# Kernel tuning notes

Hardware: AMD Instinct MI355X
Metric: run time of the kernel (lower is better)

Reference implementation:

```python
import jax, jax.numpy as jnp
import numpy as np

MID = 16
HEADS = 8
HEAD_DIM = MID // HEADS  # 2
EPS = 1e-5


def posembed(length, dim):
    # get_posembed_linear: sin-cos 1D positional embedding
    pos = jnp.arange(length, dtype=jnp.float32)
    omega = jnp.arange(dim // 2, dtype=jnp.float32) / (dim / 2.0)
    omega = 1.0 / (10000.0 ** omega)
    out = pos[:, None] * omega[None, :]  # [L, dim//2]
    return jnp.concatenate([jnp.sin(out), jnp.cos(out)], axis=1)  # [L, dim]


def layernorm(x, g, b):
    m = x.mean(-1, keepdims=True)
    v = ((x - m) ** 2).mean(-1, keepdims=True)
    return (x - m) * jax.lax.rsqrt(v + EPS) * g + b


def conv2d(x, w, b):
    # NCHW 3x3 SAME conv
    y = jax.lax.conv_general_dilated(x, w, (1, 1), 'SAME',
                                     dimension_numbers=('NCHW', 'OIHW', 'NCHW'))
    return y + b[None, :, None, None]


def attention(x, wq, wk, wv, wo, bo):
    # diffusers Attention: self-attn, no qkv bias, out bias
    B, S, C = x.shape
    q = (x @ wq.T).reshape(B, S, HEADS, HEAD_DIM)
    k = (x @ wk.T).reshape(B, S, HEADS, HEAD_DIM)
    v = (x @ wv.T).reshape(B, S, HEADS, HEAD_DIM)
    scale = 1.0 / np.sqrt(HEAD_DIM).astype(np.float32)
    scores = jnp.einsum('bshd,bthd->bhst', q, k) * scale
    p = jax.nn.softmax(scores, axis=-1)
    o = jnp.einsum('bhst,bthd->bshd', p, v).reshape(B, S, C)
    return o @ wo.T + bo


def setup_inputs() -> dict:
    key = jax.random.key(0)
    ks = jax.random.split(key, 24)

    def n(k, shape, s=0.05):
        return jax.random.normal(k, shape, dtype=jnp.float32) * s

    b, f, h, w, c = 2, 16, 64, 64, 16
    inp = {
        'hidden_states': n(ks[0], (b, f, h, w, c), 1.0),
        'ref_stats': n(ks[1], (b, f, h, w, c), 1.0),
        'emb': n(ks[2], (b, 512), 1.0),
        'conv_in_w': n(ks[3], (MID, c, 3, 3)),
        'conv_in_b': jnp.zeros((MID,), jnp.float32),
        'emb1_w': n(ks[4], (MID, 512)),
        'emb1_b': jnp.zeros((MID,), jnp.float32),
        'emb2_w': n(ks[5], (MID, MID)),
        'emb2_b': jnp.zeros((MID,), jnp.float32),
        'wqx': n(ks[6], (MID, MID)), 'wkx': n(ks[7], (MID, MID)),
        'wvx': n(ks[8], (MID, MID)), 'wox': n(ks[9], (MID, MID)),
        'box': jnp.zeros((MID,), jnp.float32),
        'wqy': n(ks[10], (MID, MID)), 'wky': n(ks[11], (MID, MID)),
        'wvy': n(ks[12], (MID, MID)), 'woy': n(ks[13], (MID, MID)),
        'boy': jnp.zeros((MID,), jnp.float32),
        'wqt': n(ks[14], (MID, MID)), 'wkt': n(ks[15], (MID, MID)),
        'wvt': n(ks[16], (MID, MID)), 'wot': n(ks[17], (MID, MID)),
        'bot': jnp.zeros((MID,), jnp.float32),
        'norm_g': jnp.ones((MID,), jnp.float32),
        'norm_b': jnp.zeros((MID,), jnp.float32),
        'proj_w': n(ks[18], (c, MID, 3, 3)),  # zero_module in torch; random here so grads flow
        'proj_b': jnp.zeros((c,), jnp.float32),
    }
    return inp


def reference(hidden_states, ref_stats, emb,
              conv_in_w, conv_in_b, emb1_w, emb1_b, emb2_w, emb2_b,
              wqx, wkx, wvx, wox, box,
              wqy, wky, wvy, woy, boy,
              wqt, wkt, wvt, wot, bot,
              norm_g, norm_b, proj_w, proj_b):
    b, f, h, w, c = hidden_states.shape

    # conv stem on (b f) c h w
    x = hidden_states.reshape(b * f, h, w, c).transpose(0, 3, 1, 2)
    x = conv2d(x, conv_in_w, conv_in_b)
    r = ref_stats.reshape(b * f, h, w, c).transpose(0, 3, 1, 2)
    r = conv2d(r, conv_in_w, conv_in_b)

    # TimestepEmbedding: linear -> silu -> linear, broadcast over frames/HW
    e = jax.nn.silu(emb @ emb1_w.T + emb1_b) @ emb2_w.T + emb2_b  # [b, MID]
    r = r + jnp.repeat(e, f, axis=0)[:, :, None, None]

    hs = x.reshape(b, f, MID, h, w).transpose(0, 1, 3, 4, 2)  # b f h w c
    rs = r.reshape(b, f, MID, h, w).transpose(0, 1, 3, 4, 2)

    # row (x) attention: cat along w -> (b f h) 2w c
    cat = jnp.concatenate([hs, rs], axis=3).reshape(b * f * h, 2 * w, MID)
    pe = posembed(2 * w, MID)
    resx = attention(layernorm(cat + pe[None], norm_g, norm_b), wqx, wkx, wvx, wox, box)
    resx = resx[:, :w].reshape(b, f, h, w, MID)

    # column (y) attention: cat along h -> (b f w) 2h c
    cat = jnp.concatenate([resx, rs], axis=2)            # b f 2h w c
    cat = cat.transpose(0, 1, 3, 2, 4).reshape(b * f * w, 2 * h, MID)
    pe = posembed(2 * h, MID)
    resy = attention(layernorm(cat + pe[None], norm_g, norm_b), wqy, wky, wvy, woy, boy)
    resy = resy[:, :h].reshape(b, f, w, h, MID).transpose(0, 1, 3, 2, 4)

    # temporal (t) attention: cat along f -> (b h w) 2f c
    cat = jnp.concatenate([resy, rs], axis=1)            # b 2f h w c
    cat = cat.transpose(0, 2, 3, 1, 4).reshape(b * h * w, 2 * f, MID)
    pe = posembed(2 * f, MID)
    rest = attention(layernorm(cat + pe[None], norm_g, norm_b), wqt, wkt, wvt, wot, bot)
    rest = rest[:, :f].reshape(b, h, w, f, MID).transpose(0, 3, 4, 1, 2).reshape(b * f, MID, h, w)

    out = conv2d(rest, proj_w, proj_b)  # (b f) c h w
    return hidden_states + out.reshape(b, f, c, h, w).transpose(0, 1, 3, 4, 2)
```

## Files before the change

kernel.cpp:

```cpp
#include <hip/hip_runtime.h>
#include <hip/hip_bf16.h>

typedef __hip_bfloat16 bf16;
using hf2 = decltype(__builtin_amdgcn_cvt_pkrtz(0.f, 0.f));

__device__ __forceinline__ float b2f(bf16 x) { return __bfloat162float(x); }

#define BB   2
#define FF   16
#define HH   64
#define WW   64
#define CC   16
#define NIMG (BB*FF)
#define PIX  (HH*WW)
#define IMGSZ (PIX*CC)

#define QSCALE_LOG2E 1.0201394f

__device__ __forceinline__ unsigned pkh2(float a, float b) {
    union { hf2 h; unsigned u; } x;
    x.h = __builtin_amdgcn_cvt_pkrtz(a, b);
    return x.u;
}
__device__ __forceinline__ float fdot2u(unsigned a, unsigned b, float c) {
    union { unsigned u; hf2 h; } A, B;
    A.u = a; B.u = b;
    return __builtin_amdgcn_fdot2(A.h, B.h, c, false);
}

__device__ __forceinline__ void ld16bf(const bf16* p, float* x) {
    const uint4* p4 = reinterpret_cast<const uint4*>(p);
    uint4 u0 = p4[0], u1 = p4[1];
    unsigned uu[8] = {u0.x, u0.y, u0.z, u0.w, u1.x, u1.y, u1.z, u1.w};
    #pragma unroll
    for (int k = 0; k < 8; ++k) {
        union { unsigned u; float f; } lo, hi;
        lo.u = uu[k] << 16;
        hi.u = uu[k] & 0xffff0000u;
        x[2 * k] = lo.f;
        x[2 * k + 1] = hi.f;
    }
}
__device__ __forceinline__ void st16bf(bf16* p, const float* x) {
    union { bf16 h[16]; uint4 u[2]; } o;
    #pragma unroll
    for (int k = 0; k < 16; ++k) o.h[k] = __float2bfloat16(x[k]);
    uint4* p4 = reinterpret_cast<uint4*>(p);
    p4[0] = o.u[0];
    p4[1] = o.u[1];
}

__device__ __forceinline__ void ld16f(const float* p, float* x) {
    const float4* p4 = reinterpret_cast<const float4*>(p);
    #pragma unroll
    for (int q = 0; q < 4; ++q) {
        float4 v = p4[q];
        x[4 * q] = v.x; x[4 * q + 1] = v.y; x[4 * q + 2] = v.z; x[4 * q + 3] = v.w;
    }
}
__device__ __forceinline__ void st16f(float* p, const float* x) {
    float4* p4 = reinterpret_cast<float4*>(p);
    #pragma unroll
    for (int q = 0; q < 4; ++q)
        p4[q] = make_float4(x[4 * q], x[4 * q + 1], x[4 * q + 2], x[4 * q + 3]);
}

__device__ __forceinline__ unsigned packbf2(float a, float b) {
    union { bf16 h[2]; unsigned u; } pk;
    pk.h[0] = __float2bfloat16(a);
    pk.h[1] = __float2bfloat16(b);
    return pk.u;
}

__global__ __launch_bounds__(256) void conv_in_kernel(
    const float* __restrict__ hid, const float* __restrict__ ref,
    const float* __restrict__ cw, const float* __restrict__ cb,
    const float* __restrict__ emb,
    const float* __restrict__ e1w, const float* __restrict__ e1b,
    const float* __restrict__ e2w, const float* __restrict__ e2b,
    bf16* __restrict__ A, bf16* __restrict__ R)
{
    __shared__ float wl[9 * 256];
    __shared__ float bl[16];
    __shared__ float hl[16];
    __shared__ float el[16];
    int t = threadIdx.x;
    {
        int ic = t >> 4, oc = t & 15;
        #pragma unroll
        for (int k = 0; k < 9; ++k)
            wl[k * 256 + t] = cw[(oc * 16 + ic) * 9 + k];
    }
    if (t < 16) bl[t] = cb[t];

    int gid  = blockIdx.x * 256 + t;
    int wi   = gid & 63;
    int hi   = (gid >> 6) & 63;
    int img2 = gid >> 12;
    int isref = img2 >> 5;
    int img  = img2 & 31;
    int bi   = img >> 4;

    if (isref) {
        if (t < 16) {
            float acc = e1b[t];
            const float* er = emb + bi * 512;
            const float* wr = e1w + t * 512;
            for (int k = 0; k < 512; ++k) acc = fmaf(er[k], wr[k], acc);
            hl[t] = acc / (1.f + __expf(-acc));
        }
        __syncthreads();
        if (t < 16) {
            float acc = e2b[t];
            #pragma unroll
            for (int k = 0; k < 16; ++k) acc = fmaf(hl[k], e2w[t * 16 + k], acc);
            el[t] = acc;
        }
    }
    __syncthreads();

    const float* inp = (isref ? ref : hid) + (size_t)img * IMGSZ;
    float acc[16];
    #pragma unroll
    for (int oc = 0; oc < 16; ++oc)
        acc[oc] = bl[oc] + (isref ? el[oc] : 0.f);

    for (int ky = 0; ky < 3; ++ky) {
        int y = hi + ky - 1;
        if ((unsigned)y >= 64u) continue;
        for (int kx = 0; kx < 3; ++kx) {
            int x = wi + kx - 1;
            if ((unsigned)x >= 64u) continue;
            float xv[16];
            ld16f(inp + (((y << 6) + x) << 4), xv);
            const float* wt = &wl[(ky * 3 + kx) * 256];
            #pragma unroll
            for (int ic = 0; ic < 16; ++ic) {
                #pragma unroll
                for (int oc = 0; oc < 16; ++oc)
                    acc[oc] = fmaf(xv[ic], wt[ic * 16 + oc], acc[oc]);
            }
        }
    }
    bf16* op = (isref ? R : A) + ((size_t)(img * PIX + (hi << 6) + wi) << 4);
    st16bf(op, acc);
}

template<int S, int SEQPB, int MINW>
__global__ __launch_bounds__(256, MINW) void attn_kernel(
    bf16* __restrict__ A, const bf16* __restrict__ R,
    int d2, int str1, int str2, int tokStride,
    const float* __restrict__ wq, const float* __restrict__ wk,
    const float* __restrict__ wv, const float* __restrict__ wo,
    const float* __restrict__ bo, const float* __restrict__ gw,
    const float* __restrict__ bw)
{
    constexpr int HS  = S / 2;
    constexpr int KQ  = S / 2;
    constexpr int TPT = 256 / (SEQPB * S);
    constexpr int NDIM = 16 / TPT;
    constexpr int ITEMS = 256 / SEQPB;
    constexpr int NQG = ITEMS / 16;
    constexpr int QB  = HS / NQG;
    constexpr int KROW = 10;
    constexpr int QROW = 20;
    constexpr int LSQ = (SEQPB == 1) ? 0 : ((SEQPB == 2) ? 1 : 2);
    constexpr int NW3 = SEQPB * HS * 8 / 256;

    __shared__ float wolT[256];
    __shared__ unsigned wq2L[128], wk2L[128], wv2L[128];
    __shared__ float bol[16], gl[16], blw[16];
    __shared__ __align__(16) unsigned kU[SEQPB * S * KROW];
    __shared__ __align__(16) unsigned vU[SEQPB * S * KROW];
    __shared__ __align__(16) unsigned qL[SEQPB * HS * KROW];
    __shared__ int bases[SEQPB];

    int t = threadIdx.x;
    wolT[(t & 15) * 16 + (t >> 4)] = wo[t];
    if (t < 128) {
        float2 qw = reinterpret_cast<const float2*>(wq)[t];
        float2 kw = reinterpret_cast<const float2*>(wk)[t];
        float2 vw = reinterpret_cast<const float2*>(wv)[t];
        wq2L[t] = pkh2(qw.x * QSCALE_LOG2E, qw.y * QSCALE_LOG2E);
        wk2L[t] = pkh2(kw.x, kw.y);
        wv2L[t] = pkh2(vw.x, vw.y);
    }
    if (t < 16) { bol[t] = bo[t]; gl[t] = gw[t]; blw[t] = bw[t]; }
    if (t < SEQPB) {
        int seq = blockIdx.x * SEQPB + t;
        bases[t] = (seq / d2) * str1 + (seq % d2) * str2;
    }
    __syncthreads();

    {
        int tokIdx = (TPT == 2) ? (t >> 1) : t;
        int db     = (TPT == 2) ? ((t & 1) * 8) : 0;
        int sq = tokIdx & (SEQPB - 1);
        int i  = tokIdx >> LSQ;
        const bf16* src = (i < HS)
            ? (A + bases[sq] + (size_t)i * tokStride)
            : (R + bases[sq] + (size_t)(i - HS) * tokStride);
        float x[16];
        ld16bf(src, x);
        const float om[8] = {1.f, 0.31622776601683794f, 0.1f, 0.031622776601683794f,
                             0.01f, 0.0031622776601683794f, 0.001f, 0.00031622776601683794f};
        float fi = (float)i;
        #pragma unroll
        for (int k = 0; k < 8; ++k) {
            float sv, cv;
            __sincosf(fi * om[k], &sv, &cv);
            x[k]     += sv;
            x[k + 8] += cv;
        }
        float m = 0.f;
        #pragma unroll
        for (int c = 0; c < 16; ++c) m += x[c];
        m *= (1.f / 16.f);
        float var = 0.f;
        #pragma unroll
        for (int c = 0; c < 16; ++c) { float d = x[c] - m; var = fmaf(d, d, var); }
        var *= (1.f / 16.f);
        float rs = rsqrtf(var + 1e-5f);
        float xn[16];
        #pragma unroll
        for (int c = 0; c < 16; ++c) xn[c] = (x[c] - m) * rs * gl[c] + blw[c];

        unsigned xp[8];
        #pragma unroll
        for (int c2 = 0; c2 < 8; ++c2) xp[c2] = pkh2(xn[2 * c2], xn[2 * c2 + 1]);

        float qv[NDIM], kv[NDIM], vv[NDIM];
        #pragma unroll
        for (int dd = 0; dd < NDIM; ++dd) {
            int d = db + dd;
            float aq = 0.f, ak = 0.f, av = 0.f;
            #pragma unroll
            for (int c2 = 0; c2 < 8; ++c2) {
                aq = fdot2u(xp[c2], wq2L[d * 8 + c2], aq);
                ak = fdot2u(xp[c2], wk2L[d * 8 + c2], ak);
                av = fdot2u(xp[c2], wv2L[d * 8 + c2], av);
            }
            qv[dd] = aq; kv[dd] = ak; vv[dd] = av;
        }
        int row = (sq * S + i) * KROW + (db >> 1);
        uint2* kr = reinterpret_cast<uint2*>(&kU[row]);
        uint2* vr = reinterpret_cast<uint2*>(&vU[row]);
        #pragma unroll
        for (int e = 0; e < NDIM / 4; ++e) {
            kr[e] = make_uint2(pkh2(kv[4 * e], kv[4 * e + 1]),
                               pkh2(kv[4 * e + 2], kv[4 * e + 3]));
            vr[e] = make_uint2(packbf2(vv[4 * e], vv[4 * e + 1]),
                               packbf2(vv[4 * e + 2], vv[4 * e + 3]));
        }
        if (i < HS) {
            uint2* qr = reinterpret_cast<uint2*>(&qL[(sq * HS + i) * KROW + (db >> 1)]);
            #pragma unroll
            for (int e = 0; e < NDIM / 4; ++e)
                qr[e] = make_uint2(pkh2(qv[4 * e], qv[4 * e + 1]),
                                   pkh2(qv[4 * e + 2], qv[4 * e + 3]));
        }
    }
    __syncthreads();

    int sq2 = t / ITEMS;
    int r   = t % ITEMS;
    int qg  = r >> 4;
    int hd  = (r >> 1) & 7;
    int half = r & 1;
    float* oL = reinterpret_cast<float*>(kU);
    {
        unsigned q2[QB];
        float l[QB], a0[QB], a1[QB];
        #pragma unroll
        for (int qq = 0; qq < QB; ++qq) {
            q2[qq] = qL[(sq2 * HS + qg * QB + qq) * KROW + hd];
            l[qq] = 0.f; a0[qq] = 0.f; a1[qq] = 0.f;
        }
        const unsigned* kp = &kU[(sq2 * S + half) * KROW + hd];
        const unsigned* vp = &vU[(sq2 * S + half) * KROW + hd];
        #pragma unroll 8
        for (int jj = 0; jj < KQ; ++jj) {
            unsigned ku = kp[jj * 2 * KROW];
            unsigned vu = vp[jj * 2 * KROW];
            union { unsigned u; float f; } v0, v1;
            v0.u = vu << 16; v1.u = vu & 0xffff0000u;
            #pragma unroll
            for (int qq = 0; qq < QB; ++qq) {
                float s = fdot2u(q2[qq], ku, 0.f);
                float p = __builtin_amdgcn_exp2f(s);
                l[qq] += p;
                a0[qq] = fmaf(p, v0.f, a0[qq]);
                a1[qq] = fmaf(p, v1.f, a1[qq]);
            }
        }
        #pragma unroll
        for (int qq = 0; qq < QB; ++qq) {
            l[qq]  += __shfl_xor(l[qq], 1);
            a0[qq] += __shfl_xor(a0[qq], 1);
            a1[qq] += __shfl_xor(a1[qq], 1);
        }
        __syncthreads();
        if (half == 0) {
            #pragma unroll
            for (int qq = 0; qq < QB; ++qq) {
                float inv = 1.f / l[qq];
                *reinterpret_cast<float2*>(
                    &oL[(sq2 * HS + qg * QB + qq) * QROW + 2 * hd]) =
                    make_float2(a0[qq] * inv, a1[qq] * inv);
            }
        }
    }
    __syncthreads();

    #pragma unroll
    for (int rep = 0; rep < NW3; ++rep) {
        int idx = t + rep * 256;
        int cp  = idx & 7;
        int g   = idx >> 3;
        int sq3 = g & (SEQPB - 1);
        int tok = g >> LSQ;
        const float* orow = &oL[(sq3 * HS + tok) * QROW];
        float acc0 = bol[2 * cp], acc1 = bol[2 * cp + 1];
        #pragma unroll
        for (int d = 0; d < 16; ++d) {
            acc0 = fmaf(orow[d], wolT[d * 16 + 2 * cp], acc0);
            acc1 = fmaf(orow[d], wolT[d * 16 + 2 * cp + 1], acc1);
        }
        *reinterpret_cast<unsigned*>(
            A + bases[sq3] + (size_t)tok * tokStride + 2 * cp) =
            packbf2(acc0, acc1);
    }
}

__global__ __launch_bounds__(256) void conv_out_kernel(
    const bf16* __restrict__ A, const float* __restrict__ hid,
    const float* __restrict__ pw, const float* __restrict__ pb,
    float* __restrict__ out)
{
    __shared__ float wl[9 * 256];
    __shared__ float bl[16];
    int t = threadIdx.x;
    {
        int ic = t >> 4, oc = t & 15;
        #pragma unroll
        for (int k = 0; k < 9; ++k)
            wl[k * 256 + t] = pw[(oc * 16 + ic) * 9 + k];
    }
    if (t < 16) bl[t] = pb[t];
    __syncthreads();

    int gid = blockIdx.x * 256 + t;
    int wi = gid & 63, hi = (gid >> 6) & 63;
    int img = gid >> 12;
    const bf16* inp = A + ((size_t)img << 16);
    float acc[16];
    #pragma unroll
    for (int oc = 0; oc < 16; ++oc) acc[oc] = bl[oc];

    for (int ky = 0; ky < 3; ++ky) {
        int y = hi + ky - 1;
        if ((unsigned)y >= 64u) continue;
        for (int kx = 0; kx < 3; ++kx) {
            int x = wi + kx - 1;
            if ((unsigned)x >= 64u) continue;
            float xv[16];
            ld16bf(inp + (((y << 6) + x) << 4), xv);
            const float* wt = &wl[(ky * 3 + kx) * 256];
            #pragma unroll
            for (int ic = 0; ic < 16; ++ic) {
                #pragma unroll
                for (int oc = 0; oc < 16; ++oc)
                    acc[oc] = fmaf(xv[ic], wt[ic * 16 + oc], acc[oc]);
            }
        }
    }
    size_t off = ((size_t)gid) << 4;
    float hv[16];
    ld16f(hid + off, hv);
    float res[16];
    #pragma unroll
    for (int k = 0; k < 16; ++k) res[k] = acc[k] + hv[k];
    st16f(out + off, res);
}

extern "C" void kernel_launch(void* const* d_in, const int* in_sizes, int n_in,
                              void* d_out, int out_size, void* d_ws, size_t ws_size,
                              hipStream_t stream) {
    const float* hid  = (const float*)d_in[0];
    const float* ref  = (const float*)d_in[1];
    const float* emb  = (const float*)d_in[2];
    const float* ciw  = (const float*)d_in[3];
    const float* cib  = (const float*)d_in[4];
    const float* e1w  = (const float*)d_in[5];
    const float* e1b  = (const float*)d_in[6];
    const float* e2w  = (const float*)d_in[7];
    const float* e2b  = (const float*)d_in[8];
    const float* wqx  = (const float*)d_in[9];
    const float* wkx  = (const float*)d_in[10];
    const float* wvx  = (const float*)d_in[11];
    const float* wox  = (const float*)d_in[12];
    const float* box_ = (const float*)d_in[13];
    const float* wqy  = (const float*)d_in[14];
    const float* wky  = (const float*)d_in[15];
    const float* wvy  = (const float*)d_in[16];
    const float* woy  = (const float*)d_in[17];
    const float* boy  = (const float*)d_in[18];
    const float* wqt  = (const float*)d_in[19];
    const float* wkt  = (const float*)d_in[20];
    const float* wvt  = (const float*)d_in[21];
    const float* wot  = (const float*)d_in[22];
    const float* bot  = (const float*)d_in[23];
    const float* ng   = (const float*)d_in[24];
    const float* nb   = (const float*)d_in[25];
    const float* pjw  = (const float*)d_in[26];
    const float* pjb  = (const float*)d_in[27];

    bf16* A = (bf16*)d_ws;
    bf16* R = (bf16*)d_out;

    conv_in_kernel<<<(2 * NIMG * PIX) / 256, 256, 0, stream>>>(
        hid, ref, ciw, cib, emb, e1w, e1b, e2w, e2b, A, R);

    attn_kernel<128, 1, 8><<<BB * FF * HH, 256, 0, stream>>>(
        A, R, 1, WW * CC, 0, CC, wqx, wkx, wvx, wox, box_, ng, nb);
    attn_kernel<128, 2, 4><<<(BB * FF * WW) / 2, 256, 0, stream>>>(
        A, R, WW, IMGSZ, CC, WW * CC, wqy, wky, wvy, woy, boy, ng, nb);
    attn_kernel<32, 4, 8><<<(BB * HH * WW) / 4, 256, 0, stream>>>(
        A, R, HH * WW, FF * IMGSZ, CC, IMGSZ, wqt, wkt, wvt, wot, bot, ng, nb);

    conv_out_kernel<<<(NIMG * PIX) / 256, 256, 0, stream>>>(A, hid, pjw, pjb, (float*)d_out);
}
```

Baseline: 249.9 us.

## Use packed fp16 dot products in convs and packed fp32 math in attention

Both 3x3 convolutions now pack weights and inputs into fp16 pairs and accumulate with fdot2, which halves the inner-loop FMA count and the LDS weight footprint. The temporal attention pass also writes its output as packed fp16 to a second workspace buffer, so conv_out loads packed pairs directly with no bf16 unpacking. The attention softmax accumulation is restructured into two-wide float vectors so the compiler can emit packed FMA/add instructions. This trades fp32 conv precision for fp16 rounding of inputs and weights, and adds an extra global store in the last attention pass.

```diff
diff --git a/kernel.cpp b/kernel.cpp
--- a/kernel.cpp
+++ b/kernel.cpp
@@ -3,6 +3,7 @@
 
 typedef __hip_bfloat16 bf16;
 using hf2 = decltype(__builtin_amdgcn_cvt_pkrtz(0.f, 0.f));
+typedef float f32x2 __attribute__((ext_vector_type(2)));
 
 __device__ __forceinline__ float b2f(bf16 x) { return __bfloat162float(x); }
 
@@ -27,6 +28,9 @@
     A.u = a; B.u = b;
     return __builtin_amdgcn_fdot2(A.h, B.h, c, false);
 }
+__device__ __forceinline__ f32x2 f2(float a, float b) {
+    f32x2 r; r.x = a; r.y = b; return r;
+}
 
 __device__ __forceinline__ void ld16bf(const bf16* p, float* x) {
     const uint4* p4 = reinterpret_cast<const uint4*>(p);
@@ -80,16 +84,18 @@
     const float* __restrict__ e2w, const float* __restrict__ e2b,
     bf16* __restrict__ A, bf16* __restrict__ R)
 {
-    __shared__ float wl[9 * 256];
+    __shared__ unsigned w2l[9 * 128];
     __shared__ float bl[16];
     __shared__ float hl[16];
     __shared__ float el[16];
     int t = threadIdx.x;
-    {
-        int ic = t >> 4, oc = t & 15;
+    if (t < 128) {
+        int oc = t & 15, c2 = t >> 4;
         #pragma unroll
         for (int k = 0; k < 9; ++k)
-            wl[k * 256 + t] = cw[(oc * 16 + ic) * 9 + k];
+            w2l[k * 128 + oc * 8 + c2] =
+                pkh2(cw[(oc * 16 + 2 * c2) * 9 + k],
+                     cw[(oc * 16 + 2 * c2 + 1) * 9 + k]);
     }
     if (t < 16) bl[t] = cb[t];
 
@@ -133,12 +139,18 @@
             if ((unsigned)x >= 64u) continue;
             float xv[16];
             ld16f(inp + (((y << 6) + x) << 4), xv);
-            const float* wt = &wl[(ky * 3 + kx) * 256];
-            #pragma unroll
-            for (int ic = 0; ic < 16; ++ic) {
+            unsigned xp[8];
+            #pragma unroll
+            for (int c2 = 0; c2 < 8; ++c2)
+                xp[c2] = pkh2(xv[2 * c2], xv[2 * c2 + 1]);
+            const unsigned* wt = &w2l[(ky * 3 + kx) * 128];
+            #pragma unroll
+            for (int oc = 0; oc < 16; ++oc) {
+                float a = acc[oc];
                 #pragma unroll
-                for (int oc = 0; oc < 16; ++oc)
-                    acc[oc] = fmaf(xv[ic], wt[ic * 16 + oc], acc[oc]);
+                for (int c2 = 0; c2 < 8; ++c2)
+                    a = fdot2u(xp[c2], wt[oc * 8 + c2], a);
+                acc[oc] = a;
             }
         }
     }
@@ -146,9 +158,10 @@
     st16bf(op, acc);
 }
 
-template<int S, int SEQPB, int MINW>
+template<int S, int SEQPB, int MINW, bool F16OUT>
 __global__ __launch_bounds__(256, MINW) void attn_kernel(
     bf16* __restrict__ A, const bf16* __restrict__ R,
+    unsigned* __restrict__ A16,
     int d2, int str1, int str2, int tokStride,
     const float* __restrict__ wq, const float* __restrict__ wk,
     const float* __restrict__ wv, const float* __restrict__ wo,
@@ -162,6 +175,7 @@
     constexpr int ITEMS = 256 / SEQPB;
     constexpr int NQG = ITEMS / 16;
     constexpr int QB  = HS / NQG;
+    constexpr int QP  = QB / 2;
     constexpr int KROW = 10;
     constexpr int QROW = 20;
     constexpr int LSQ = (SEQPB == 1) ? 0 : ((SEQPB == 2) ? 1 : 2);
@@ -270,11 +284,13 @@
     float* oL = reinterpret_cast<float*>(kU);
     {
         unsigned q2[QB];
-        float l[QB], a0[QB], a1[QB];
-        #pragma unroll
-        for (int qq = 0; qq < QB; ++qq) {
+        f32x2 l2[QP], a0p[QP], a1p[QP];
+        #pragma unroll
+        for (int qq = 0; qq < QB; ++qq)
             q2[qq] = qL[(sq2 * HS + qg * QB + qq) * KROW + hd];
-            l[qq] = 0.f; a0[qq] = 0.f; a1[qq] = 0.f;
+        #pragma unroll
+        for (int m = 0; m < QP; ++m) {
+            l2[m] = f2(0.f, 0.f); a0p[m] = f2(0.f, 0.f); a1p[m] = f2(0.f, 0.f);
         }
         const unsigned* kp = &kU[(sq2 * S + half) * KROW + hd];
         const unsigned* vp = &vU[(sq2 * S + half) * KROW + hd];
@@ -284,29 +300,36 @@
             unsigned vu = vp[jj * 2 * KROW];
             union { unsigned u; float f; } v0, v1;
             v0.u = vu << 16; v1.u = vu & 0xffff0000u;
-            #pragma unroll
-            for (int qq = 0; qq < QB; ++qq) {
-                float s = fdot2u(q2[qq], ku, 0.f);
-                float p = __builtin_amdgcn_exp2f(s);
-                l[qq] += p;
-                a0[qq] = fmaf(p, v0.f, a0[qq]);
-                a1[qq] = fmaf(p, v1.f, a1[qq]);
+            f32x2 v00 = f2(v0.f, v0.f);
+            f32x2 v11 = f2(v1.f, v1.f);
+            #pragma unroll
+            for (int m = 0; m < QP; ++m) {
+                f32x2 p2;
+                p2.x = __builtin_amdgcn_exp2f(fdot2u(q2[2 * m], ku, 0.f));
+                p2.y = __builtin_amdgcn_exp2f(fdot2u(q2[2 * m + 1], ku, 0.f));
+                l2[m] += p2;
+                a0p[m] = __builtin_elementwise_fma(p2, v00, a0p[m]);
+                a1p[m] = __builtin_elementwise_fma(p2, v11, a1p[m]);
             }
         }
         #pragma unroll
-        for (int qq = 0; qq < QB; ++qq) {
-            l[qq]  += __shfl_xor(l[qq], 1);
-            a0[qq] += __shfl_xor(a0[qq], 1);
-            a1[qq] += __shfl_xor(a1[qq], 1);
+        for (int m = 0; m < QP; ++m) {
+            l2[m].x  += __shfl_xor(l2[m].x, 1);  l2[m].y  += __shfl_xor(l2[m].y, 1);
+            a0p[m].x += __shfl_xor(a0p[m].x, 1); a0p[m].y += __shfl_xor(a0p[m].y, 1);
+            a1p[m].x += __shfl_xor(a1p[m].x, 1); a1p[m].y += __shfl_xor(a1p[m].y, 1);
         }
         __syncthreads();
         if (half == 0) {
             #pragma unroll
-            for (int qq = 0; qq < QB; ++qq) {
-                float inv = 1.f / l[qq];
+            for (int m = 0; m < QP; ++m) {
+                float inv0 = 1.f / l2[m].x;
+                float inv1 = 1.f / l2[m].y;
                 *reinterpret_cast<float2*>(
-                    &oL[(sq2 * HS + qg * QB + qq) * QROW + 2 * hd]) =
-                    make_float2(a0[qq] * inv, a1[qq] * inv);
+                    &oL[(sq2 * HS + qg * QB + 2 * m) * QROW + 2 * hd]) =
+                    make_float2(a0p[m].x * inv0, a1p[m].x * inv0);
+                *reinterpret_cast<float2*>(
+                    &oL[(sq2 * HS + qg * QB + 2 * m + 1) * QROW + 2 * hd]) =
+                    make_float2(a0p[m].y * inv1, a1p[m].y * inv1);
             }
         }
     }
@@ -326,25 +349,28 @@
             acc0 = fmaf(orow[d], wolT[d * 16 + 2 * cp], acc0);
             acc1 = fmaf(orow[d], wolT[d * 16 + 2 * cp + 1], acc1);
         }
-        *reinterpret_cast<unsigned*>(
-            A + bases[sq3] + (size_t)tok * tokStride + 2 * cp) =
-            packbf2(acc0, acc1);
+        int off = bases[sq3] + tok * tokStride;
+        *reinterpret_cast<unsigned*>(A + off + 2 * cp) = packbf2(acc0, acc1);
+        if constexpr (F16OUT)
+            A16[(off >> 1) + cp] = pkh2(acc0, acc1);
     }
 }
 
 __global__ __launch_bounds__(256) void conv_out_kernel(
-    const bf16* __restrict__ A, const float* __restrict__ hid,
+    const unsigned* __restrict__ A16, const float* __restrict__ hid,
     const float* __restrict__ pw, const float* __restrict__ pb,
     float* __restrict__ out)
 {
-    __shared__ float wl[9 * 256];
+    __shared__ unsigned w2l[9 * 128];
     __shared__ float bl[16];
     int t = threadIdx.x;
-    {
-        int ic = t >> 4, oc = t & 15;
+    if (t < 128) {
+        int oc = t & 15, c2 = t >> 4;
         #pragma unroll
         for (int k = 0; k < 9; ++k)
-            wl[k * 256 + t] = pw[(oc * 16 + ic) * 9 + k];
+            w2l[k * 128 + oc * 8 + c2] =
+                pkh2(pw[(oc * 16 + 2 * c2) * 9 + k],
+                     pw[(oc * 16 + 2 * c2 + 1) * 9 + k]);
     }
     if (t < 16) bl[t] = pb[t];
     __syncthreads();
@@ -352,7 +378,7 @@
     int gid = blockIdx.x * 256 + t;
     int wi = gid & 63, hi = (gid >> 6) & 63;
     int img = gid >> 12;
-    const bf16* inp = A + ((size_t)img << 16);
+    const unsigned* inp = A16 + ((size_t)img << 15);
     float acc[16];
     #pragma unroll
     for (int oc = 0; oc < 16; ++oc) acc[oc] = bl[oc];
@@ -363,14 +389,18 @@
         for (int kx = 0; kx < 3; ++kx) {
             int x = wi + kx - 1;
             if ((unsigned)x >= 64u) continue;
-            float xv[16];
-            ld16bf(inp + (((y << 6) + x) << 4), xv);
-            const float* wt = &wl[(ky * 3 + kx) * 256];
-            #pragma unroll
-            for (int ic = 0; ic < 16; ++ic) {
+            const uint4* p4 = reinterpret_cast<const uint4*>(
+                inp + (((y << 6) + x) << 3));
+            uint4 u0 = p4[0], u1 = p4[1];
+            unsigned xp[8] = {u0.x, u0.y, u0.z, u0.w, u1.x, u1.y, u1.z, u1.w};
+            const unsigned* wt = &w2l[(ky * 3 + kx) * 128];
+            #pragma unroll
+            for (int oc = 0; oc < 16; ++oc) {
+                float a = acc[oc];
                 #pragma unroll
-                for (int oc = 0; oc < 16; ++oc)
-                    acc[oc] = fmaf(xv[ic], wt[ic * 16 + oc], acc[oc]);
+                for (int c2 = 0; c2 < 8; ++c2)
+                    a = fdot2u(xp[c2], wt[oc * 8 + c2], a);
+                acc[oc] = a;
             }
         }
     }
@@ -416,17 +446,18 @@
     const float* pjb  = (const float*)d_in[27];
 
     bf16* A = (bf16*)d_ws;
+    unsigned* A16 = (unsigned*)((char*)d_ws + (4 << 20));
     bf16* R = (bf16*)d_out;
 
     conv_in_kernel<<<(2 * NIMG * PIX) / 256, 256, 0, stream>>>(
         hid, ref, ciw, cib, emb, e1w, e1b, e2w, e2b, A, R);
 
-    attn_kernel<128, 1, 8><<<BB * FF * HH, 256, 0, stream>>>(
-        A, R, 1, WW * CC, 0, CC, wqx, wkx, wvx, wox, box_, ng, nb);
-    attn_kernel<128, 2, 4><<<(BB * FF * WW) / 2, 256, 0, stream>>>(
-        A, R, WW, IMGSZ, CC, WW * CC, wqy, wky, wvy, woy, boy, ng, nb);
-    attn_kernel<32, 4, 8><<<(BB * HH * WW) / 4, 256, 0, stream>>>(
-        A, R, HH * WW, FF * IMGSZ, CC, IMGSZ, wqt, wkt, wvt, wot, bot, ng, nb);
-
-    conv_out_kernel<<<(NIMG * PIX) / 256, 256, 0, stream>>>(A, hid, pjw, pjb, (float*)d_out);
-}
+    attn_kernel<128, 1, 8, false><<<BB * FF * HH, 256, 0, stream>>>(
+        A, R, nullptr, 1, WW * CC, 0, CC, wqx, wkx, wvx, wox, box_, ng, nb);
+    attn_kernel<128, 2, 4, false><<<(BB * FF * WW) / 2, 256, 0, stream>>>(
+        A, R, nullptr, WW, IMGSZ, CC, WW * CC, wqy, wky, wvy, woy, boy, ng, nb);
+    attn_kernel<32, 4, 8, true><<<(BB * HH * WW) / 4, 256, 0, stream>>>(
+        A, R, A16, HH * WW, FF * IMGSZ, CC, IMGSZ, wqt, wkt, wvt, wot, bot, ng, nb);
+
+    conv_out_kernel<<<(NIMG * PIX) / 256, 256, 0, stream>>>(A16, hid, pjw, pjb, (float*)d_out);
+}
```

Result: faster. 243.1 us (-2.7%).
